# Optimization experiments

Hardware: AMD Instinct MI355X
Metric: run time of the kernel (lower is better)

Reference implementation:

```python
import jax, jax.numpy as jnp
import numpy as np

B, H, W, D = 4, 64, 64, 384
M, P = 12, 9
DH = D // M             # 32 head dim
DFF = 3 * D             # 1152 FFN hidden
N = H * W               # 4096 queries (single level)


def setup_inputs():
    key = jax.random.key(0)
    ks = jax.random.split(key, 12)
    g = lambda k, s, sc=0.02: jax.random.normal(k, s, jnp.float32) * sc
    return {
        "x": jax.random.normal(ks[0], (B, D, H, W), jnp.float32),
        "qry_masks": jnp.zeros((B, H, W), jnp.float32),
        "so_w": g(ks[1], (M * P * 2, D)), "so_b": g(ks[2], (M * P * 2,)),
        "aw_w": g(ks[3], (M * P, D)), "aw_b": g(ks[4], (M * P,)),
        "vp_w": g(ks[5], (D, D)), "vp_b": jnp.zeros((D,), jnp.float32),
        "op_w": g(ks[6], (D, D)), "op_b": jnp.zeros((D,), jnp.float32),
        "ln1_g": jnp.ones((D,), jnp.float32), "ln1_b": jnp.zeros((D,), jnp.float32),
        "w1": g(ks[7], (DFF, D)), "w2": g(ks[8], (D, DFF)),
        "ln2_g": jnp.ones((D,), jnp.float32), "ln2_b": jnp.zeros((D,), jnp.float32),
        "level_embed": g(ks[9], (1, D), 1.0),
    }


def _layernorm(x, g, b, eps=1e-5):
    mu = x.mean(-1, keepdims=True)
    v = ((x - mu) ** 2).mean(-1, keepdims=True)
    return (x - mu) * jax.lax.rsqrt(v + eps) * g + b


def _sine_pos(mask):
    # mask: [B,H,W] bool. mmdet SinePositionalEncoding(num_feats=D//2, normalize=True)
    not_mask = (~mask).astype(jnp.float32)
    y = jnp.cumsum(not_mask, 1)
    x = jnp.cumsum(not_mask, 2)
    eps, scale = 1e-6, 2.0 * np.pi
    y = y / (y[:, -1:, :] + eps) * scale
    x = x / (x[:, :, -1:] + eps) * scale
    nf = D // 2
    dim_t = 10000.0 ** (2.0 * (jnp.arange(nf) // 2).astype(jnp.float32) / nf)
    px, py = x[..., None] / dim_t, y[..., None] / dim_t

    def interleave(p):
        return jnp.stack([jnp.sin(p[..., 0::2]), jnp.cos(p[..., 1::2])], -1).reshape(p.shape[:-1] + (nf,))

    return jnp.concatenate([interleave(py), interleave(px)], -1)  # [B,H,W,D]


def _bilinear_gather(v, px, py):
    # v: [B,M,HW,DH]; px,py: [B,M,NP] pixel coords (grid_sample align_corners=False, zero pad)
    x0 = jnp.floor(px); y0 = jnp.floor(py)
    lx, ly = px - x0, py - y0
    x0i, y0i = x0.astype(jnp.int32), y0.astype(jnp.int32)
    out = jnp.zeros(v.shape[:2] + (px.shape[-1], v.shape[-1]), v.dtype)
    for dx, dy, wgt in ((0, 0, (1 - lx) * (1 - ly)), (1, 0, lx * (1 - ly)),
                        (0, 1, (1 - lx) * ly), (1, 1, lx * ly)):
        xi, yi = x0i + dx, y0i + dy
        valid = ((xi >= 0) & (xi < W) & (yi >= 0) & (yi < H)).astype(v.dtype)
        idx = jnp.clip(yi, 0, H - 1) * W + jnp.clip(xi, 0, W - 1)
        g = jnp.take_along_axis(v, idx[..., None], axis=2)  # [B,M,NP,DH]
        out = out + (wgt * valid)[..., None] * g
    return out


def _msdeform_attn(q, value_in, ref, mask_flat,
                   so_w, so_b, aw_w, aw_b, vp_w, vp_b, op_w, op_b):
    value = value_in @ vp_w.T + vp_b                      # [B,N,D]
    value = jnp.where(mask_flat[..., None], 0.0, value)
    so = (q @ so_w.T + so_b).reshape(B, N, M, P, 2)       # single level
    aw = jax.nn.softmax((q @ aw_w.T + aw_b).reshape(B, N, M, P), axis=-1)
    norm = jnp.array([W, H], jnp.float32)
    loc = ref[:, :, None, None, :] + so / norm            # [B,N,M,P,2] in [0,1]
    v = value.reshape(B, N, M, DH).transpose(0, 2, 1, 3)  # [B,M,HW,DH]
    px = (loc[..., 0] * W - 0.5).transpose(0, 2, 1, 3).reshape(B, M, N * P)
    py = (loc[..., 1] * H - 0.5).transpose(0, 2, 1, 3).reshape(B, M, N * P)
    sampled = _bilinear_gather(v, px, py).reshape(B, M, N, P, DH)
    out = jnp.einsum('bmnpd,bnmp->bnmd', sampled, aw).reshape(B, N, D)
    return out @ op_w.T + op_b


def reference(x, qry_masks, so_w, so_b, aw_w, aw_b, vp_w, vp_b, op_w, op_b,
              ln1_g, ln1_b, w1, w2, ln2_g, ln2_b, level_embed):
    mask = (qry_masks == 255.0)                           # [B,H,W] bool
    pos = _sine_pos(mask).reshape(B, N, D) + level_embed[0]
    src = x.reshape(B, D, N).transpose(0, 2, 1)           # [B,N,D]
    mask_flat = mask.reshape(B, N)
    gy, gx = jnp.meshgrid((jnp.arange(H, dtype=jnp.float32) + 0.5) / H,
                          (jnp.arange(W, dtype=jnp.float32) + 0.5) / W, indexing='ij')
    ref = jnp.stack([gx.reshape(-1), gy.reshape(-1)], -1)[None]  # [1,N,2] (x,y)
    q = src
    attn = _msdeform_attn(q + pos, q, ref, mask_flat,
                          so_w, so_b, aw_w, aw_b, vp_w, vp_b, op_w, op_b)
    q = _layernorm(q + attn, ln1_g, ln1_b)
    q = _layernorm(q + jax.nn.relu(q @ w1.T) @ w2.T, ln2_g, ln2_b)
    return q.transpose(0, 2, 1).reshape(B, D, H, W)
```

## Files before the change

kernel.cpp:

```cpp
#include <hip/hip_runtime.h>
#include <math.h>

#define Bc   4
#define Hc   64
#define Wc   64
#define Dc   384
#define Nc   4096
#define Mc   12
#define Pc   9
#define DHc  32
#define DFFc 1152
#define BNc  (Bc*Nc)

typedef __attribute__((ext_vector_type(8))) short short8;
typedef __attribute__((ext_vector_type(4))) float floatx4;

__device__ __forceinline__ ushort f2bf(float f) {
    union { float f; unsigned u; } v; v.f = f;
    unsigned r = v.u + 0x7fffu + ((v.u >> 16) & 1u);
    return (ushort)(r >> 16);
}
__device__ __forceinline__ float bf2f(ushort u) {
    union { unsigned u; float f; } v; v.u = (unsigned)u << 16; return v.f;
}

__device__ __forceinline__ void gload_lds16(const void* g, void* l) {
    __builtin_amdgcn_global_load_lds(
        (const __attribute__((address_space(1))) void*)(uintptr_t)g,
        (__attribute__((address_space(3))) void*)(uintptr_t)l,
        16, 0, 0);
}

#define SOW_N  82944
#define AWW_N  41472
#define VPW_N  147456
#define OPW_N  147456
#define W1_N   442368
#define W2_N   442368
#define WTOT   1304064

__global__ void init_kernel(const float* __restrict__ so_w,
                            const float* __restrict__ aw_w,
                            const float* __restrict__ vp_w,
                            const float* __restrict__ op_w,
                            const float* __restrict__ w1,
                            const float* __restrict__ w2,
                            const float* __restrict__ so_b,
                            const float* __restrict__ aw_b,
                            ushort* __restrict__ out,
                            float* __restrict__ bias_out) {
    int i = blockIdx.x * 256 + threadIdx.x;
    if (i < WTOT) {
        float v;
        int j = i;
        if (j < SOW_N) v = so_w[j];
        else if ((j -= SOW_N) < AWW_N) v = aw_w[j];
        else if ((j -= AWW_N) < VPW_N) v = vp_w[j];
        else if ((j -= VPW_N) < OPW_N) v = op_w[j];
        else if ((j -= OPW_N) < W1_N)  v = w1[j];
        else { j -= W1_N; v = w2[j]; }
        out[i] = f2bf(v);
        return;
    }
    int j = i - WTOT;
    if (j < 384) {
        bias_out[j] = (j < 216) ? so_b[j] : (j < 324 ? aw_b[j - 216] : 0.f);
    }
}

__global__ __launch_bounds__(256) void cumsum_kernel(
        const float* __restrict__ qmask,
        float* __restrict__ cum_y, float* __restrict__ cum_x) {
    __shared__ float nm[64 * 65];
    __shared__ float ot[64 * 65];
    int b = blockIdx.x;
    int t = threadIdx.x;
    const float* qm = qmask + b * 4096;
    #pragma unroll
    for (int k = 0; k < 16; ++k) {
        int idx = t + k * 256;
        nm[(idx >> 6) * 65 + (idx & 63)] = (qm[idx] == 255.0f) ? 0.f : 1.f;
    }
    __syncthreads();
    if (t < 64) {
        float run = 0.f;
        for (int h = 0; h < 64; ++h) { run += nm[h * 65 + t]; ot[h * 65 + t] = run; }
    }
    __syncthreads();
    #pragma unroll
    for (int k = 0; k < 16; ++k) {
        int idx = t + k * 256;
        cum_y[b * 4096 + idx] = ot[(idx >> 6) * 65 + (idx & 63)];
    }
    __syncthreads();
    if (t < 64) {
        float run = 0.f;
        for (int w = 0; w < 64; ++w) { run += nm[t * 65 + w]; ot[t * 65 + w] = run; }
    }
    __syncthreads();
    #pragma unroll
    for (int k = 0; k < 16; ++k) {
        int idx = t + k * 256;
        cum_x[b * 4096 + idx] = ot[(idx >> 6) * 65 + (idx & 63)];
    }
}

__global__ void transpose_pos_kernel(const float* __restrict__ x,
                                     const float* __restrict__ cum_y,
                                     const float* __restrict__ cum_x,
                                     const float* __restrict__ level_embed,
                                     ushort* __restrict__ src_bf,
                                     ushort* __restrict__ qpos_bf) {
    __shared__ float tile[32][33];
    int b  = blockIdx.z;
    int n0 = blockIdx.x * 32, d0 = blockIdx.y * 32;
    int tx = threadIdx.x, ty = threadIdx.y;
    tile[ty][tx] = x[((size_t)b * Dc + (d0 + ty)) * Nc + (n0 + tx)];
    __syncthreads();
    int n = n0 + ty, d = d0 + tx;
    float v = tile[tx][ty];
    size_t oi = ((size_t)b * Nc + n) * Dc + d;
    src_bf[oi] = f2bf(v);
    int h = n >> 6, w = n & 63;
    const float TWO_PI = 6.28318530717958647692f;
    float vy = cum_y[(b * Hc + h) * Wc + w] /
               (cum_y[(b * Hc + (Hc - 1)) * Wc + w] + 1e-6f) * TWO_PI;
    float vx = cum_x[(b * Hc + h) * Wc + w] /
               (cum_x[(b * Hc + h) * Wc + (Wc - 1)] + 1e-6f) * TWO_PI;
    int   i  = (d < 192) ? d : d - 192;
    float vv = (d < 192) ? vy : vx;
    float e   = (float)(i >> 1) * (2.0f / 192.0f);
    float idt = exp2f(e * -13.28771237954945f);
    float ang = vv * idt;
    float pe  = (i & 1) ? __cosf(ang) : __sinf(ang);
    qpos_bf[oi] = f2bf(v + pe + level_embed[d]);
}

template <int KT>
__device__ __forceinline__ void gemm_core(
        const ushort* __restrict__ A, const ushort* __restrict__ Wt,
        const float* __restrict__ bias,
        float* __restrict__ Cf, ushort* __restrict__ Cb,
        int Nout, int relu, const float* __restrict__ qmask,
        ushort* As, ushort* Bs) {
    constexpr int NCH = KT / 32;
    const int tid  = threadIdx.x;
    const int m0   = blockIdx.x * 128;
    const int n0   = blockIdx.y * 128;
    const int lane = tid & 63;
    const int wv   = tid >> 6;
    const int wr   = (wv >> 1) * 64;
    const int wc   = (wv & 1) * 64;
    const int quad = lane >> 4;
    const int lrow = lane & 15;
    const int srow = wv * 32 + (lane >> 2);
    const int scol = (lane & 3) * 8;

    floatx4 acc[4][4];
    #pragma unroll
    for (int i = 0; i < 4; ++i)
        #pragma unroll
        for (int j = 0; j < 4; ++j)
            acc[i][j] = (floatx4)(0.f);

    #pragma unroll
    for (int s = 0; s < 2; ++s) {
        gload_lds16(A  + (size_t)(m0 + srow + s * 16) * KT + scol,
                    As + wv * 1024 + s * 512);
        gload_lds16(Wt + (size_t)(n0 + srow + s * 16) * KT + scol,
                    Bs + wv * 1024 + s * 512);
    }

    for (int c = 0; c < NCH; ++c) {
        const int cur = c & 1;
        __syncthreads();
        if (c + 1 < NCH) {
            const int k0 = (c + 1) * 32;
            #pragma unroll
            for (int s = 0; s < 2; ++s) {
                gload_lds16(A  + (size_t)(m0 + srow + s * 16) * KT + k0 + scol,
                            As + (cur ^ 1) * 4096 + wv * 1024 + s * 512);
                gload_lds16(Wt + (size_t)(n0 + srow + s * 16) * KT + k0 + scol,
                            Bs + (cur ^ 1) * 4096 + wv * 1024 + s * 512);
            }
        }
        short8 afr[4], bfr[4];
        #pragma unroll
        for (int i = 0; i < 4; ++i)
            afr[i] = *(const short8*)(As + cur * 4096 +
                                      (wr + i * 16 + lrow) * 32 + quad * 8);
        #pragma unroll
        for (int j = 0; j < 4; ++j)
            bfr[j] = *(const short8*)(Bs + cur * 4096 +
                                      (wc + j * 16 + lrow) * 32 + quad * 8);
        #pragma unroll
        for (int i = 0; i < 4; ++i)
            #pragma unroll
            for (int j = 0; j < 4; ++j)
                acc[i][j] = __builtin_amdgcn_mfma_f32_16x16x32_bf16(
                    afr[i], bfr[j], acc[i][j], 0, 0, 0);
    }

    float mz[4][4];
    #pragma unroll
    for (int i = 0; i < 4; ++i)
        #pragma unroll
        for (int r = 0; r < 4; ++r) {
            int row = m0 + wr + i * 16 + quad * 4 + r;
            mz[i][r] = (qmask && qmask[row] == 255.0f) ? 0.f : 1.f;
        }

    #pragma unroll
    for (int i = 0; i < 4; ++i) {
        #pragma unroll
        for (int j = 0; j < 4; ++j) {
            int col = n0 + wc + j * 16 + lrow;
            if (col >= Nout) continue;
            float bsv = bias ? bias[col] : 0.f;
            #pragma unroll
            for (int r = 0; r < 4; ++r) {
                int row = m0 + wr + i * 16 + quad * 4 + r;
                float v = acc[i][j][r] + bsv;
                if (relu) v = fmaxf(v, 0.f);
                v *= mz[i][r];
                if (Cf) Cf[(size_t)row * Nout + col] = v;
                if (Cb) Cb[(size_t)row * Nout + col] = f2bf(v);
            }
        }
    }
}

template <int KT>
__global__ __launch_bounds__(256) void gemm_single_kernel(
        const ushort* __restrict__ A, const ushort* __restrict__ Wt,
        const float* __restrict__ bias,
        float* __restrict__ Cf, ushort* __restrict__ Cb,
        int Nout, int relu, const float* __restrict__ qmask) {
    __shared__ ushort As[2 * 128 * 32];
    __shared__ ushort Bs[2 * 128 * 32];
    gemm_core<KT>(A, Wt, bias, Cf, Cb, Nout, relu, qmask, As, Bs);
}

__global__ __launch_bounds__(256) void gemm_dual_kernel(
        const ushort* __restrict__ A0, const ushort* __restrict__ W0,
        const float* __restrict__ b0, float* __restrict__ Cf0,
        const ushort* __restrict__ A1, const ushort* __restrict__ W1,
        const float* __restrict__ b1, ushort* __restrict__ Cb1,
        const float* __restrict__ qmask) {
    __shared__ ushort As[2 * 128 * 32];
    __shared__ ushort Bs[2 * 128 * 32];
    if (blockIdx.z == 0)
        gemm_core<384>(A0, W0, b0, Cf0, nullptr, 384, 0, nullptr, As, Bs);
    else
        gemm_core<384>(A1, W1, b1, nullptr, Cb1, 384, 0, qmask, As, Bs);
}

template <int KT, int MODE>
__global__ __launch_bounds__(512) void gemm_fullrow_kernel(
        const ushort* __restrict__ A, const ushort* __restrict__ Wt,
        const float* __restrict__ bias, const void* __restrict__ resid,
        const float* __restrict__ g, const float* __restrict__ beta,
        float* __restrict__ outf, ushort* __restrict__ outb) {
    constexpr int NCH = KT / 32;
    __shared__ ushort As[4 * 2048];
    __shared__ ushort Bs[4 * 12288];
    __shared__ float eps1[8][64], eps2[8][64];
    __shared__ float mu_l[64], rs_l[64];
    const int tid  = threadIdx.x;
    const int lane = tid & 63;
    const int wv   = tid >> 6;
    const int quad = lane >> 4;
    const int lrow = lane & 15;
    const int m0   = blockIdx.x * 64;
    const int srow = lane >> 2;
    const int scol = (lane & 3) * 8;

    floatx4 acc[4][3];
    #pragma unroll
    for (int i = 0; i < 4; ++i)
        #pragma unroll
        for (int j = 0; j < 3; ++j)
            acc[i][j] = (floatx4)(0.f);

#define STAGE_CHUNK(c, buf)                                                   \
    {   const int k0_ = (c) * 32;                                             \
        if (wv < 4)                                                           \
            gload_lds16(A + (size_t)(m0 + wv * 16 + srow) * KT + k0_ + scol,  \
                        As + (buf) * 2048 + wv * 512);                        \
        _Pragma("unroll")                                                     \
        for (int s_ = 0; s_ < 3; ++s_)                                        \
            gload_lds16(Wt + (size_t)(wv * 48 + s_ * 16 + srow) * KT + k0_ + scol, \
                        Bs + (buf) * 12288 + wv * 1536 + s_ * 512);           \
    }

    STAGE_CHUNK(0, 0)
    STAGE_CHUNK(1, 1)
    STAGE_CHUNK(2, 2)

    #pragma unroll
    for (int c = 0; c < NCH; ++c) {
        const int rem = (NCH - 1 - c) >= 2 ? 2 : (NCH - 1 - c);
        if (wv < 4) {
            if (rem == 2)      asm volatile("s_waitcnt vmcnt(8)" ::: "memory");
            else if (rem == 1) asm volatile("s_waitcnt vmcnt(4)" ::: "memory");
            else               asm volatile("s_waitcnt vmcnt(0)" ::: "memory");
        } else {
            if (rem == 2)      asm volatile("s_waitcnt vmcnt(6)" ::: "memory");
            else if (rem == 1) asm volatile("s_waitcnt vmcnt(3)" ::: "memory");
            else               asm volatile("s_waitcnt vmcnt(0)" ::: "memory");
        }
        __builtin_amdgcn_s_barrier();
        __builtin_amdgcn_sched_barrier(0);
        if (c + 3 < NCH) { STAGE_CHUNK(c + 3, (c + 3) & 3) }
        const int buf = c & 3;
        short8 afr[4], bfr[3];
        #pragma unroll
        for (int i = 0; i < 4; ++i)
            afr[i] = *(const short8*)(As + buf * 2048 +
                                      (i * 16 + lrow) * 32 + quad * 8);
        #pragma unroll
        for (int j = 0; j < 3; ++j)
            bfr[j] = *(const short8*)(Bs + buf * 12288 +
                                      (wv * 48 + j * 16 + lrow) * 32 + quad * 8);
        #pragma unroll
        for (int i = 0; i < 4; ++i)
            #pragma unroll
            for (int j = 0; j < 3; ++j)
                acc[i][j] = __builtin_amdgcn_mfma_f32_16x16x32_bf16(
                    afr[i], bfr[j], acc[i][j], 0, 0, 0);
    }
#undef STAGE_CHUNK

    float s1[16], s2[16];
    #pragma unroll
    for (int k = 0; k < 16; ++k) { s1[k] = 0.f; s2[k] = 0.f; }
    #pragma unroll
    for (int i = 0; i < 4; ++i) {
        #pragma unroll
        for (int r = 0; r < 4; ++r) {
            int rl = i * 16 + quad * 4 + r;
            #pragma unroll
            for (int j = 0; j < 3; ++j) {
                int col = wv * 48 + j * 16 + lrow;
                float t = acc[i][j][r];
                if (bias) t += bias[col];
                if (MODE == 0)
                    t += bf2f(((const ushort*)resid)[(size_t)(m0 + rl) * Dc + col]);
                else
                    t += ((const float*)resid)[(size_t)(m0 + rl) * Dc + col];
                acc[i][j][r] = t;
                s1[i * 4 + r] += t;
                s2[i * 4 + r] += t * t;
            }
        }
    }
    #pragma unroll
    for (int mm = 1; mm < 16; mm <<= 1) {
        #pragma unroll
        for (int k = 0; k < 16; ++k) {
            s1[k] += __shfl_xor(s1[k], mm);
            s2[k] += __shfl_xor(s2[k], mm);
        }
    }
    if (lrow == 0) {
        #pragma unroll
        for (int i = 0; i < 4; ++i)
            #pragma unroll
            for (int r = 0; r < 4; ++r) {
                int rl = i * 16 + quad * 4 + r;
                eps1[wv][rl] = s1[i * 4 + r];
                eps2[wv][rl] = s2[i * 4 + r];
            }
    }
    __syncthreads();
    if (tid < 64) {
        float a1 = 0.f, a2 = 0.f;
        #pragma unroll
        for (int w = 0; w < 8; ++w) { a1 += eps1[w][tid]; a2 += eps2[w][tid]; }
        float mu  = a1 * (1.0f / Dc);
        float var = a2 * (1.0f / Dc) - mu * mu;
        mu_l[tid] = mu;
        rs_l[tid] = rsqrtf(var + 1e-5f);
    }
    __syncthreads();

    #pragma unroll
    for (int i = 0; i < 4; ++i) {
        #pragma unroll
        for (int r = 0; r < 4; ++r) {
            int rl = i * 16 + quad * 4 + r;
            float mu = mu_l[rl], rs = rs_l[rl];
            #pragma unroll
            for (int j = 0; j < 3; ++j) {
                int col = wv * 48 + j * 16 + lrow;
                acc[i][j][r] = (acc[i][j][r] - mu) * rs * g[col] + beta[col];
            }
        }
    }

    if (MODE == 0) {
        #pragma unroll
        for (int i = 0; i < 4; ++i)
            #pragma unroll
            for (int j = 0; j < 3; ++j) {
                int col = wv * 48 + j * 16 + lrow;
                #pragma unroll
                for (int r = 0; r < 4; ++r) {
                    int rl = i * 16 + quad * 4 + r;
                    float v = acc[i][j][r];
                    outf[(size_t)(m0 + rl) * Dc + col] = v;
                    outb[(size_t)(m0 + rl) * Dc + col] = f2bf(v);
                }
            }
    } else {
        float* tile = (float*)Bs;
        const int b   = m0 >> 12;
        const int n0r = m0 & 4095;
        #pragma unroll
        for (int gp = 0; gp < 2; ++gp) {
            __syncthreads();
            if ((wv >> 2) == gp) {
                int cbase = (wv & 3) * 48;
                #pragma unroll
                for (int i = 0; i < 4; ++i)
                    #pragma unroll
                    for (int j = 0; j < 3; ++j) {
                        int c = cbase + j * 16 + lrow;
                        #pragma unroll
                        for (int r = 0; r < 4; ++r) {
                            int rl = i * 16 + quad * 4 + r;
                            tile[rl * 193 + c] = acc[i][j][r];
                        }
                    }
            }
            __syncthreads();
            const int row = tid & 63;
            const int cp  = tid >> 6;
            #pragma unroll
            for (int it = 0; it < 24; ++it) {
                int c = it * 8 + cp;
                outf[((size_t)(b * Dc + gp * 192 + c)) * Nc + n0r + row] =
                    tile[row * 193 + c];
            }
        }
    }
}

__global__ __launch_bounds__(256) void deform_attn_kernel(
        const ushort* __restrict__ value_bf, const float* __restrict__ soaw,
        ushort* __restrict__ out) {
    int bid   = blockIdx.x;
    int slice = bid % 48;
    int h     = bid / 48;
    int m  = slice % Mc;
    int b  = slice / Mc;
    int w  = threadIdx.x >> 2;
    int l4 = threadIdx.x & 3;
    int n  = (h << 6) | w;
    int bn = b * Nc + n;
    const float* sop = soaw + (size_t)bn * 384 + m * 18;
    const float* lgt = soaw + (size_t)bn * 384 + 216 + m * Pc;
    float awv[Pc];
    float mx = lgt[0];
    #pragma unroll
    for (int i = 1; i < Pc; ++i) mx = fmaxf(mx, lgt[i]);
    float ssum = 0.f;
    #pragma unroll
    for (int i = 0; i < Pc; ++i) { awv[i] = __expf(lgt[i] - mx); ssum += awv[i]; }
    float sinv = 1.f / ssum;
    const ushort* vb = value_bf + ((size_t)b * Nc) * Dc + m * DHc + l4 * 8;
    float acc[8] = {0.f, 0.f, 0.f, 0.f, 0.f, 0.f, 0.f, 0.f};
    #pragma unroll
    for (int p = 0; p < Pc; ++p) {
        float2 so2 = *(const float2*)(sop + p * 2);
        float px = (float)w + so2.x;
        float py = (float)h + so2.y;
        float x0f = floorf(px), y0f = floorf(py);
        float lx = px - x0f, ly = py - y0f;
        int x0 = (int)x0f, y0 = (int)y0f;
        int x1 = x0 + 1,  y1 = y0 + 1;
        float a = awv[p] * sinv;
        float w00 = (1.f - lx) * (1.f - ly) * a;
        float w01 = lx * (1.f - ly) * a;
        float w10 = (1.f - lx) * ly * a;
        float w11 = lx * ly * a;
        bool bx0 = (unsigned)x0 < 64u, bx1 = (unsigned)x1 < 64u;
        bool by0 = (unsigned)y0 < 64u, by1 = (unsigned)y1 < 64u;
        w00 = (bx0 && by0) ? w00 : 0.f;
        w01 = (bx1 && by0) ? w01 : 0.f;
        w10 = (bx0 && by1) ? w10 : 0.f;
        w11 = (bx1 && by1) ? w11 : 0.f;
        int cx0 = min(max(x0, 0), 63), cx1 = min(max(x1, 0), 63);
        int cy0 = min(max(y0, 0), 63), cy1 = min(max(y1, 0), 63);
        uint4 q00 = *(const uint4*)(vb + (size_t)(cy0 * 64 + cx0) * Dc);
        uint4 q01 = *(const uint4*)(vb + (size_t)(cy0 * 64 + cx1) * Dc);
        uint4 q10 = *(const uint4*)(vb + (size_t)(cy1 * 64 + cx0) * Dc);
        uint4 q11 = *(const uint4*)(vb + (size_t)(cy1 * 64 + cx1) * Dc);
        union { unsigned u; float f; } t;
        #define ACC2(word, wg, k)                                   \
            t.u = (word) << 16;         acc[k]     += (wg) * t.f;   \
            t.u = (word) & 0xffff0000u; acc[k + 1] += (wg) * t.f;
        #define ACC8(q, wg) \
            ACC2((q).x, wg, 0) ACC2((q).y, wg, 2) ACC2((q).z, wg, 4) ACC2((q).w, wg, 6)
        ACC8(q00, w00) ACC8(q01, w01) ACC8(q10, w10) ACC8(q11, w11)
        #undef ACC8
        #undef ACC2
    }
    short8 o;
    #pragma unroll
    for (int k = 0; k < 8; ++k) o[k] = (short)f2bf(acc[k]);
    *(short8*)(out + (size_t)bn * Dc + m * DHc + l4 * 8) = o;
}

extern "C" void kernel_launch(void* const* d_in, const int* in_sizes, int n_in,
                              void* d_out, int out_size, void* d_ws, size_t ws_size,
                              hipStream_t stream) {
    (void)in_sizes; (void)n_in; (void)out_size; (void)ws_size;
    const float* x      = (const float*)d_in[0];
    const float* qmask  = (const float*)d_in[1];
    const float* so_w   = (const float*)d_in[2];
    const float* so_b   = (const float*)d_in[3];
    const float* aw_w   = (const float*)d_in[4];
    const float* aw_b   = (const float*)d_in[5];
    const float* vp_w   = (const float*)d_in[6];
    const float* vp_b   = (const float*)d_in[7];
    const float* op_w   = (const float*)d_in[8];
    const float* op_b   = (const float*)d_in[9];
    const float* ln1_g  = (const float*)d_in[10];
    const float* ln1_b  = (const float*)d_in[11];
    const float* w1     = (const float*)d_in[12];
    const float* w2     = (const float*)d_in[13];
    const float* ln2_g  = (const float*)d_in[14];
    const float* ln2_b  = (const float*)d_in[15];
    const float* lvl    = (const float*)d_in[16];
    float* out = (float*)d_out;

    float*  ws       = (float*)d_ws;
    float*  q1_f     = ws;
    ushort* src_bf   = (ushort*)(q1_f + 6291456);
    ushort* qpos_bf  = src_bf + 6291456;
    ushort* value_bf = qpos_bf + 6291456;
    ushort* hbuf_bf  = value_bf + 6291456;
    float*  soaw_f   = (float*)hbuf_bf;
    ushort* wbuf     = hbuf_bf + 18874368;
    float*  soaw_bias= (float*)(wbuf + 1304064);
    float*  cum_y    = soaw_bias + 384;
    float*  cum_x    = cum_y + 16384;

    const ushort* soaw_wb = wbuf;
    const ushort* vp_wb = soaw_wb + SOW_N + AWW_N;
    const ushort* op_wb = vp_wb + VPW_N;
    const ushort* w1_b  = op_wb + OPW_N;
    const ushort* w2_b  = w1_b + W1_N;

    init_kernel<<<(WTOT + 384 + 255) / 256, 256, 0, stream>>>(
        so_w, aw_w, vp_w, op_w, w1, w2, so_b, aw_b, wbuf, soaw_bias);
    cumsum_kernel<<<Bc, 256, 0, stream>>>(qmask, cum_y, cum_x);
    transpose_pos_kernel<<<dim3(Nc / 32, Dc / 32, Bc), dim3(32, 32), 0, stream>>>(
        x, cum_y, cum_x, lvl, src_bf, qpos_bf);
    gemm_dual_kernel<<<dim3(BNc / 128, 3, 2), 256, 0, stream>>>(
        qpos_bf, soaw_wb, soaw_bias, soaw_f,
        src_bf, vp_wb, vp_b, value_bf, qmask);
    deform_attn_kernel<<<3072, 256, 0, stream>>>(
        value_bf, soaw_f, qpos_bf);
    gemm_fullrow_kernel<384, 0><<<BNc / 64, 512, 0, stream>>>(
        qpos_bf, op_wb, op_b, src_bf, ln1_g, ln1_b, q1_f, qpos_bf);
    gemm_single_kernel<384><<<dim3(BNc / 128, 9), 256, 0, stream>>>(
        qpos_bf, w1_b, nullptr, nullptr, hbuf_bf, DFFc, 1, nullptr);
    gemm_fullrow_kernel<1152, 1><<<BNc / 64, 512, 0, stream>>>(
        hbuf_bf, w2_b, nullptr, q1_f, ln2_g, ln2_b, out, nullptr);
}
```

Baseline: 269.7 us.

## Fuse FFN up-projection, ReLU, down-projection and LayerNorm into one kernel

Replaces the separate W1 GEMM and the W2+LayerNorm kernel with a single kernel per 64-row tile. It computes the 1152-wide hidden activation in 128-column chunks, keeps each chunk in shared memory as bf16 and accumulates the W2 product in registers. This removes the global write and read of the large hidden buffer and one kernel launch. In exchange it uses about 139KB of LDS per block, which limits occupancy, and relies on hand-tuned vmcnt waits whose correctness depends on the exact order in which loads are issued.

New measurement: 259.4 us. 1.04x faster.

```diff
diff --git a/kernel.cpp b/kernel.cpp
--- a/kernel.cpp
+++ b/kernel.cpp
@@ -230,17 +230,6 @@
     }
 }
 
-template <int KT>
-__global__ __launch_bounds__(256) void gemm_single_kernel(
-        const ushort* __restrict__ A, const ushort* __restrict__ Wt,
-        const float* __restrict__ bias,
-        float* __restrict__ Cf, ushort* __restrict__ Cb,
-        int Nout, int relu, const float* __restrict__ qmask) {
-    __shared__ ushort As[2 * 128 * 32];
-    __shared__ ushort Bs[2 * 128 * 32];
-    gemm_core<KT>(A, Wt, bias, Cf, Cb, Nout, relu, qmask, As, Bs);
-}
-
 __global__ __launch_bounds__(256) void gemm_dual_kernel(
         const ushort* __restrict__ A0, const ushort* __restrict__ W0,
         const float* __restrict__ b0, float* __restrict__ Cf0,
@@ -255,7 +244,7 @@
         gemm_core<384>(A1, W1, b1, nullptr, Cb1, 384, 0, qmask, As, Bs);
 }
 
-template <int KT, int MODE>
+template <int KT>
 __global__ __launch_bounds__(512) void gemm_fullrow_kernel(
         const ushort* __restrict__ A, const ushort* __restrict__ Wt,
         const float* __restrict__ bias, const void* __restrict__ resid,
@@ -344,10 +333,7 @@
                 int col = wv * 48 + j * 16 + lrow;
                 float t = acc[i][j][r];
                 if (bias) t += bias[col];
-                if (MODE == 0)
-                    t += bf2f(((const ushort*)resid)[(size_t)(m0 + rl) * Dc + col]);
-                else
-                    t += ((const float*)resid)[(size_t)(m0 + rl) * Dc + col];
+                t += bf2f(((const ushort*)resid)[(size_t)(m0 + rl) * Dc + col]);
                 acc[i][j][r] = t;
                 s1[i * 4 + r] += t;
                 s2[i * 4 + r] += t * t;
@@ -383,7 +369,6 @@
         rs_l[tid] = rsqrtf(var + 1e-5f);
     }
     __syncthreads();
-
     #pragma unroll
     for (int i = 0; i < 4; ++i) {
         #pragma unroll
@@ -393,55 +378,235 @@
             #pragma unroll
             for (int j = 0; j < 3; ++j) {
                 int col = wv * 48 + j * 16 + lrow;
-                acc[i][j][r] = (acc[i][j][r] - mu) * rs * g[col] + beta[col];
-            }
-        }
-    }
-
-    if (MODE == 0) {
+                float v = (acc[i][j][r] - mu) * rs * g[col] + beta[col];
+                outf[(size_t)(m0 + rl) * Dc + col] = v;
+                outb[(size_t)(m0 + rl) * Dc + col] = f2bf(v);
+            }
+        }
+    }
+}
+
+__global__ __launch_bounds__(512) void ffn_fused_kernel(
+        const ushort* __restrict__ A,
+        const ushort* __restrict__ W1b,
+        const ushort* __restrict__ W2b,
+        const float* __restrict__ resid,
+        const float* __restrict__ g, const float* __restrict__ beta,
+        float* __restrict__ outf) {
+    __shared__ ushort smem[69632];
+    ushort* Ast = smem;
+    ushort* Hs  = smem + 24576;
+    ushort* W1s = smem + 32768;
+    ushort* W2s = smem + 45056;
+    __shared__ float eps1[8][64], eps2[8][64];
+    __shared__ float mu_l[64], rs_l[64];
+
+    const int tid  = threadIdx.x;
+    const int lane = tid & 63;
+    const int wv   = tid >> 6;
+    const int quad = lane >> 4;
+    const int lrow = lane & 15;
+    const int m0   = blockIdx.x * 64;
+    const int srow = lane >> 2;
+    const int scol = (lane & 3) * 8;
+
+    ushort* W1w = W1s + wv * 1536;
+    ushort* W2w = W2s + wv * 3072;
+
+    floatx4 acc2[4][3];
+    #pragma unroll
+    for (int i = 0; i < 4; ++i)
+        #pragma unroll
+        for (int j = 0; j < 3; ++j)
+            acc2[i][j] = (floatx4)(0.f);
+
+#define STAGE_W1(hcv, kcv, buf)                                               \
+    gload_lds16(W1b + (size_t)((hcv) * 128 + wv * 16 + srow) * 384 + (kcv) * 32 + scol, \
+                W1w + (buf) * 512 + lane * 8);
+
+#define STAGE_W2(hcv, kc2v, buf)                                              \
+    _Pragma("unroll")                                                         \
+    for (int s_ = 0; s_ < 3; ++s_)                                            \
+        gload_lds16(W2b + (size_t)(wv * 48 + s_ * 16 + srow) * 1152 + (hcv) * 128 + (kc2v) * 32 + scol, \
+                    W2w + (buf) * 1536 + s_ * 512 + lane * 8);
+
+    #pragma unroll
+    for (int k = 0; k < 6; ++k) {
+        int l   = tid + 512 * k;
+        int kc_ = l >> 8;
+        int rem = l & 255;
+        gload_lds16(A + (size_t)(m0 + (rem >> 2)) * 384 + kc_ * 32 + (rem & 3) * 8,
+                    Ast + l * 8);
+    }
+    STAGE_W1(0, 0, 0)
+    STAGE_W1(0, 1, 1)
+    asm volatile("s_waitcnt vmcnt(2)" ::: "memory");
+    __builtin_amdgcn_sched_barrier(0);
+    __builtin_amdgcn_s_barrier();
+    __builtin_amdgcn_sched_barrier(0);
+
+    floatx4 acc1[4];
+    for (int hc = 0; hc < 9; ++hc) {
+        #pragma unroll
+        for (int i = 0; i < 4; ++i) acc1[i] = (floatx4)(0.f);
+
+        #pragma unroll
+        for (int kc = 0; kc < 12; ++kc) {
+            if (kc < 10)      { STAGE_W1(hc, kc + 2, (kc + 2) % 3) }
+            else if (kc == 10){ STAGE_W2(hc, 0, 0) }
+            else              { STAGE_W2(hc, 1, 1) }
+            if (kc < 10)       asm volatile("s_waitcnt vmcnt(2)" ::: "memory");
+            else if (kc == 10) asm volatile("s_waitcnt vmcnt(4)" ::: "memory");
+            else               asm volatile("s_waitcnt vmcnt(6)" ::: "memory");
+            short8 afr[4], bfr;
+            #pragma unroll
+            for (int i = 0; i < 4; ++i)
+                afr[i] = *(const short8*)(Ast + kc * 2048 +
+                                          (i * 16 + lrow) * 32 + quad * 8);
+            bfr = *(const short8*)(W1w + (kc % 3) * 512 + lrow * 32 + quad * 8);
+            #pragma unroll
+            for (int i = 0; i < 4; ++i)
+                acc1[i] = __builtin_amdgcn_mfma_f32_16x16x32_bf16(
+                    afr[i], bfr, acc1[i], 0, 0, 0);
+        }
+
         #pragma unroll
         for (int i = 0; i < 4; ++i)
+            #pragma unroll
+            for (int r = 0; r < 4; ++r) {
+                int row = i * 16 + quad * 4 + r;
+                Hs[(wv >> 1) * 2048 + row * 32 + (wv & 1) * 16 + lrow] =
+                    f2bf(fmaxf(acc1[i][r], 0.f));
+            }
+        asm volatile("s_waitcnt lgkmcnt(0)" ::: "memory");
+        __builtin_amdgcn_sched_barrier(0);
+        __builtin_amdgcn_s_barrier();
+        __builtin_amdgcn_sched_barrier(0);
+
+        #pragma unroll
+        for (int kc2 = 0; kc2 < 4; ++kc2) {
+            if (kc2 == 0)      asm volatile("s_waitcnt vmcnt(3)" ::: "memory");
+            else if (kc2 == 1) asm volatile("s_waitcnt vmcnt(4)" ::: "memory");
+            else if (kc2 == 2) asm volatile("s_waitcnt vmcnt(5)" ::: "memory");
+            else               asm volatile("s_waitcnt vmcnt(1)" ::: "memory");
+            short8 afr[4], bfr[3];
+            #pragma unroll
+            for (int i = 0; i < 4; ++i)
+                afr[i] = *(const short8*)(Hs + kc2 * 2048 +
+                                          (i * 16 + lrow) * 32 + quad * 8);
+            #pragma unroll
+            for (int j = 0; j < 3; ++j)
+                bfr[j] = *(const short8*)(W2w + (kc2 & 1) * 1536 +
+                                          (j * 16 + lrow) * 32 + quad * 8);
+            asm volatile("s_waitcnt lgkmcnt(0)" ::: "memory");
+            __builtin_amdgcn_sched_barrier(0);
+            if (kc2 == 0)      { STAGE_W2(hc, 2, 0) STAGE_W1(hc + 1, 0, 0) }
+            else if (kc2 == 1) { STAGE_W2(hc, 3, 1) STAGE_W1(hc + 1, 1, 1) }
+            #pragma unroll
+            for (int i = 0; i < 4; ++i)
+                #pragma unroll
+                for (int j = 0; j < 3; ++j)
+                    acc2[i][j] = __builtin_amdgcn_mfma_f32_16x16x32_bf16(
+                        afr[i], bfr[j], acc2[i][j], 0, 0, 0);
+        }
+        asm volatile("s_waitcnt lgkmcnt(0)" ::: "memory");
+        __builtin_amdgcn_sched_barrier(0);
+        __builtin_amdgcn_s_barrier();
+        __builtin_amdgcn_sched_barrier(0);
+    }
+    asm volatile("s_waitcnt vmcnt(0)" ::: "memory");
+#undef STAGE_W1
+#undef STAGE_W2
+
+    float s1[16], s2[16];
+    #pragma unroll
+    for (int k = 0; k < 16; ++k) { s1[k] = 0.f; s2[k] = 0.f; }
+    #pragma unroll
+    for (int i = 0; i < 4; ++i) {
+        #pragma unroll
+        for (int r = 0; r < 4; ++r) {
+            int rl = i * 16 + quad * 4 + r;
             #pragma unroll
             for (int j = 0; j < 3; ++j) {
                 int col = wv * 48 + j * 16 + lrow;
+                float t = acc2[i][j][r];
+                t += resid[(size_t)(m0 + rl) * Dc + col];
+                acc2[i][j][r] = t;
+                s1[i * 4 + r] += t;
+                s2[i * 4 + r] += t * t;
+            }
+        }
+    }
+    #pragma unroll
+    for (int mm = 1; mm < 16; mm <<= 1) {
+        #pragma unroll
+        for (int k = 0; k < 16; ++k) {
+            s1[k] += __shfl_xor(s1[k], mm);
+            s2[k] += __shfl_xor(s2[k], mm);
+        }
+    }
+    if (lrow == 0) {
+        #pragma unroll
+        for (int i = 0; i < 4; ++i)
+            #pragma unroll
+            for (int r = 0; r < 4; ++r) {
+                int rl = i * 16 + quad * 4 + r;
+                eps1[wv][rl] = s1[i * 4 + r];
+                eps2[wv][rl] = s2[i * 4 + r];
+            }
+    }
+    __syncthreads();
+    if (tid < 64) {
+        float a1 = 0.f, a2 = 0.f;
+        #pragma unroll
+        for (int w = 0; w < 8; ++w) { a1 += eps1[w][tid]; a2 += eps2[w][tid]; }
+        float mu  = a1 * (1.0f / Dc);
+        float var = a2 * (1.0f / Dc) - mu * mu;
+        mu_l[tid] = mu;
+        rs_l[tid] = rsqrtf(var + 1e-5f);
+    }
+    __syncthreads();
+    #pragma unroll
+    for (int i = 0; i < 4; ++i) {
+        #pragma unroll
+        for (int r = 0; r < 4; ++r) {
+            int rl = i * 16 + quad * 4 + r;
+            float mu = mu_l[rl], rs = rs_l[rl];
+            #pragma unroll
+            for (int j = 0; j < 3; ++j) {
+                int col = wv * 48 + j * 16 + lrow;
+                acc2[i][j][r] = (acc2[i][j][r] - mu) * rs * g[col] + beta[col];
+            }
+        }
+    }
+    float* tile = (float*)smem;
+    const int b   = m0 >> 12;
+    const int n0r = m0 & 4095;
+    #pragma unroll
+    for (int gp = 0; gp < 2; ++gp) {
+        __syncthreads();
+        if ((wv >> 2) == gp) {
+            int cbase = (wv & 3) * 48;
+            #pragma unroll
+            for (int i = 0; i < 4; ++i)
                 #pragma unroll
-                for (int r = 0; r < 4; ++r) {
-                    int rl = i * 16 + quad * 4 + r;
-                    float v = acc[i][j][r];
-                    outf[(size_t)(m0 + rl) * Dc + col] = v;
-                    outb[(size_t)(m0 + rl) * Dc + col] = f2bf(v);
+                for (int j = 0; j < 3; ++j) {
+                    int c = cbase + j * 16 + lrow;
+                    #pragma unroll
+                    for (int r = 0; r < 4; ++r) {
+                        int rl = i * 16 + quad * 4 + r;
+                        tile[rl * 193 + c] = acc2[i][j][r];
+                    }
                 }
-            }
-    } else {
-        float* tile = (float*)Bs;
-        const int b   = m0 >> 12;
-        const int n0r = m0 & 4095;
-        #pragma unroll
-        for (int gp = 0; gp < 2; ++gp) {
-            __syncthreads();
-            if ((wv >> 2) == gp) {
-                int cbase = (wv & 3) * 48;
-                #pragma unroll
-                for (int i = 0; i < 4; ++i)
-                    #pragma unroll
-                    for (int j = 0; j < 3; ++j) {
-                        int c = cbase + j * 16 + lrow;
-                        #pragma unroll
-                        for (int r = 0; r < 4; ++r) {
-                            int rl = i * 16 + quad * 4 + r;
-                            tile[rl * 193 + c] = acc[i][j][r];
-                        }
-                    }
-            }
-            __syncthreads();
-            const int row = tid & 63;
-            const int cp  = tid >> 6;
-            #pragma unroll
-            for (int it = 0; it < 24; ++it) {
-                int c = it * 8 + cp;
-                outf[((size_t)(b * Dc + gp * 192 + c)) * Nc + n0r + row] =
-                    tile[row * 193 + c];
-            }
+        }
+        __syncthreads();
+        const int row = tid & 63;
+        const int cp  = tid >> 6;
+        #pragma unroll
+        for (int it = 0; it < 24; ++it) {
+            int c = it * 8 + cp;
+            outf[((size_t)(b * Dc + gp * 192 + c)) * Nc + n0r + row] =
+                tile[row * 193 + c];
         }
     }
 }
@@ -563,10 +728,8 @@
         src_bf, vp_wb, vp_b, value_bf, qmask);
     deform_attn_kernel<<<3072, 256, 0, stream>>>(
         value_bf, soaw_f, qpos_bf);
-    gemm_fullrow_kernel<384, 0><<<BNc / 64, 512, 0, stream>>>(
+    gemm_fullrow_kernel<384><<<BNc / 64, 512, 0, stream>>>(
         qpos_bf, op_wb, op_b, src_bf, ln1_g, ln1_b, q1_f, qpos_bf);
-    gemm_single_kernel<384><<<dim3(BNc / 128, 9), 256, 0, stream>>>(
-        qpos_bf, w1_b, nullptr, nullptr, hbuf_bf, DFFc, 1, nullptr);
-    gemm_fullrow_kernel<1152, 1><<<BNc / 64, 512, 0, stream>>>(
-        hbuf_bf, w2_b, nullptr, q1_f, ln2_g, ln2_b, out, nullptr);
-}
+    ffn_fused_kernel<<<BNc / 64, 512, 0, stream>>>(
+        qpos_bf, w1_b, w2_b, q1_f, ln2_g, ln2_b, out);
+}
```
